# Performance work log

Measured on AMD Instinct MI355X. Metric: run time of the kernel, lower is better.

## Reference

```python
import jax, jax.numpy as jnp
import numpy as np

N, E = 100000, 1600000
IN, H, OUT = 128, 128, 64
LN_EPS = 1e-5


def _prep(edge_index, n):
    # Add self loops (PyG GCNConv default) and compute symmetric normalization.
    loops = jnp.arange(n)
    src = jnp.concatenate([edge_index[0], loops])
    dst = jnp.concatenate([edge_index[1], loops])
    deg = jax.ops.segment_sum(jnp.ones_like(dst, dtype=jnp.float32), dst, num_segments=n)
    dinv = jax.lax.rsqrt(jnp.maximum(deg, 1.0))  # deg >= 1 due to self loops
    return src, dst, dinv


def _gcn_conv(x, W, b, src, dst, dinv, n):
    h = x @ W                                   # [N, F_out] dense transform
    coef = dinv[src] * dinv[dst]                # [E+N] symmetric norm
    msg = h[src] * coef[:, None]                # gather + scale
    out = jax.ops.segment_sum(msg, dst, num_segments=n)  # scatter-add
    return out + b


def _layer_norm(x, g, b):
    mu = jnp.mean(x, axis=-1, keepdims=True)
    var = jnp.mean(jnp.square(x - mu), axis=-1, keepdims=True)
    return (x - mu) * jax.lax.rsqrt(var + LN_EPS) * g + b


def setup_inputs() -> dict:
    key = jax.random.key(0)
    ks = jax.random.split(key, 8)
    return {
        "x": jax.random.normal(ks[0], (N, IN), dtype=jnp.float32),
        "edge_index": jax.random.randint(ks[1], (2, E), 0, N),
        "W1": jax.random.normal(ks[2], (IN, H), dtype=jnp.float32) / np.sqrt(IN).astype(np.float32),
        "b1": jnp.zeros((H,), jnp.float32),
        "g1": jnp.ones((H,), jnp.float32),
        "be1": jnp.zeros((H,), jnp.float32),
        "W2": jax.random.normal(ks[3], (H, H), dtype=jnp.float32) / np.sqrt(H).astype(np.float32),
        "b2": jnp.zeros((H,), jnp.float32),
        "g2": jnp.ones((H,), jnp.float32),
        "be2": jnp.zeros((H,), jnp.float32),
        "W3": jax.random.normal(ks[4], (H, OUT), dtype=jnp.float32) / np.sqrt(H).astype(np.float32),
        "b3": jnp.zeros((OUT,), jnp.float32),
    }


def reference(x, edge_index, W1, b1, g1, be1, W2, b2, g2, be2, W3, b3):
    n = x.shape[0]
    src, dst, dinv = _prep(edge_index, n)
    h = _gcn_conv(x, W1, b1, src, dst, dinv, n)
    h = jax.nn.relu(_layer_norm(h, g1, be1))
    h = _gcn_conv(h, W2, b2, src, dst, dinv, n)
    h = jax.nn.relu(_layer_norm(h, g2, be2))
    return _gcn_conv(h, W3, b3, src, dst, dinv, n)
```

## Files before the change

### kernel.cpp

```cpp
#include <hip/hip_runtime.h>

using short8 = __attribute__((ext_vector_type(8))) short;
using f32x4  = __attribute__((ext_vector_type(4))) float;

#define BSHIFT 9
#define BSIZE  512
#define CAP    12288
#define CHUNK  2048


__device__ __forceinline__ float bf_lo(unsigned int v) {
    return __int_as_float((int)(v << 16));
}
__device__ __forceinline__ float bf_hi(unsigned int v) {
    return __int_as_float((int)(v & 0xffff0000u));
}
__device__ __forceinline__ unsigned int f2bf(float f) {
    unsigned int x = __float_as_uint(f);
    x += 0x7fffu + ((x >> 16) & 1u);
    return x >> 16;
}
__device__ __forceinline__ unsigned int pack_bf2(float lo, float hi) {
    return f2bf(lo) | (f2bf(hi) << 16);
}


__global__ void wconv_kernel(const float* __restrict__ W1, const float* __restrict__ W2,
                             const float* __restrict__ W3, unsigned short* __restrict__ o1,
                             unsigned short* __restrict__ o2, unsigned short* __restrict__ o3) {
    int i = blockIdx.x * 256 + threadIdx.x;
    const float* W;
    unsigned short* o;
    int ncol, j;
    if (i < 16384)      { W = W1; o = o1; ncol = 128; j = i; }
    else if (i < 32768) { W = W2; o = o2; ncol = 128; j = i - 16384; }
    else if (i < 40960) { W = W3; o = o3; ncol = 64;  j = i - 32768; }
    else return;
    int k = j / ncol, c = j % ncol;
    int byte = (c * 256 + k * 2) ^ ((c & 7) << 4);
    o[byte >> 1] = (unsigned short)f2bf(W[j]);
}


__global__ __launch_bounds__(256) void bin_kernel(
    const int* __restrict__ src, const int* __restrict__ dst, int E,
    int2* __restrict__ region, int* __restrict__ bfill) {
    __shared__ int lcnt[256];
    __shared__ int loff[256];
    __shared__ int gbase[256];
    __shared__ int2 stage[CHUNK];
    __shared__ unsigned short bOf[CHUNK];

    int t = threadIdx.x;
    int e0 = blockIdx.x * CHUNK;
    int cnt = min(CHUNK, E - e0);

    lcnt[t] = 0;
    __syncthreads();

    int s_[8], d_[8], p_[8];
#pragma unroll
    for (int i = 0; i < 8; i++) {
        int e = t + i * 256;
        if (e < cnt) {
            int s = src[e0 + e], d = dst[e0 + e];
            s_[i] = s;
            d_[i] = d;
            p_[i] = atomicAdd(&lcnt[d >> BSHIFT], 1);
        } else {
            d_[i] = -1;
        }
    }
    __syncthreads();

    int v = lcnt[t];
    loff[t] = v;
    __syncthreads();
    for (int off = 1; off < 256; off <<= 1) {
        int u = (t >= off) ? loff[t - off] : 0;
        __syncthreads();
        loff[t] += u;
        __syncthreads();
    }
    int ex = loff[t] - v;
    __syncthreads();
    loff[t] = ex;
    gbase[t] = (v > 0) ? atomicAdd(&bfill[t], v) : 0;
    __syncthreads();

#pragma unroll
    for (int i = 0; i < 8; i++) {
        if (d_[i] >= 0) {
            int b = d_[i] >> BSHIFT;
            int j = loff[b] + p_[i];
            stage[j] = make_int2(s_[i], d_[i]);
            bOf[j] = (unsigned short)b;
        }
    }
    __syncthreads();

    for (int j = t; j < cnt; j += 256) {
        int b = bOf[j];
        int idx = gbase[b] + (j - loff[b]);
        if (idx < CAP) region[(size_t)b * CAP + idx] = stage[j];
    }
}

__global__ void bscan_kernel(const int* __restrict__ bfill, int* __restrict__ bbase,
                             int* __restrict__ row_ptr, int nbuck, int n) {
    __shared__ int sh[256];
    int t = threadIdx.x;
    int v = (t < nbuck) ? min(bfill[t], CAP) : 0;
    sh[t] = v;
    __syncthreads();
    for (int off = 1; off < 256; off <<= 1) {
        int u = (t >= off) ? sh[t - off] : 0;
        __syncthreads();
        sh[t] += u;
        __syncthreads();
    }
    if (t < nbuck) bbase[t] = sh[t] - v;
    if (t == nbuck - 1) row_ptr[n] = sh[t];
}

__global__ __launch_bounds__(512) void build_kernel(
    const int2* __restrict__ region, const int* __restrict__ bfill,
    const int* __restrict__ bbase, int* __restrict__ row_ptr, float* __restrict__ dinv,
    int* __restrict__ col, int n) {
    __shared__ int cnt[BSIZE];
    __shared__ int excl[BSIZE];
    __shared__ int fill[BSIZE];
    int b = blockIdx.x;
    int t = threadIdx.x;
    int base = b * BSIZE;
    int ecnt = min(bfill[b], CAP);
    int ebase = bbase[b];
    const int2* reg = region + (size_t)b * CAP;

    cnt[t] = 0;
    fill[t] = 0;
    __syncthreads();

    for (int i = t; i < ecnt; i += 512) atomicAdd(&cnt[reg[i].y - base], 1);
    __syncthreads();

    int v = cnt[t];
    excl[t] = v;
    __syncthreads();
    for (int off = 1; off < 512; off <<= 1) {
        int u = (t >= off) ? excl[t - off] : 0;
        __syncthreads();
        excl[t] += u;
        __syncthreads();
    }
    int ex = excl[t] - v;
    __syncthreads();
    excl[t] = ex;
    __syncthreads();

    int node = base + t;
    if (node < n) {
        row_ptr[node] = ebase + ex;
        dinv[node] = rsqrtf((float)(v + 1));
    }

    for (int i = t; i < ecnt; i += 512) {
        int2 sd = reg[i];
        int li = sd.y - base;
        int pos = atomicAdd(&fill[li], 1);
        col[ebase + excl[li] + pos] = sd.x;
    }
}


template <int NCOL, bool XF32>
__global__ __launch_bounds__(256) void mfma_gemm_kernel(const void* __restrict__ Xv,
                                                        const unsigned short* __restrict__ Wsw,
                                                        const float* __restrict__ dinv,
                                                        unsigned int* __restrict__ Y, int n) {
    constexpr int CF = NCOL / 16;
    __shared__ unsigned short Wt[(size_t)NCOL * 128];

    int t = threadIdx.x;
    {
        const uint4* Wg = (const uint4*)Wsw;
        uint4* Wl = (uint4*)Wt;
        for (int i = t; i < NCOL * 16; i += 256) Wl[i] = Wg[i];
    }
    __syncthreads();

    int wid = t >> 6, l = t & 63;
    int row0 = blockIdx.x * 128;
    int kq = l >> 4;
    const char* Wb = (const char*)Wt;

    for (int rt = 0; rt < 2; rt++) {
        int xr = row0 + (wid * 2 + rt) * 16 + (l & 15);
        int xrc = min(xr, n - 1);

        f32x4 acc[CF];
#pragma unroll
        for (int cf = 0; cf < CF; cf++) acc[cf] = (f32x4){0.f, 0.f, 0.f, 0.f};

#pragma unroll
        for (int ks = 0; ks < 4; ks++) {
            short8 bq;
            if (XF32) {
                const float* Xf = (const float*)Xv + (size_t)xrc * 128 + ks * 32 + kq * 8;
                float4 x0 = ((const float4*)Xf)[0];
                float4 x1 = ((const float4*)Xf)[1];
                unsigned int p0 = pack_bf2(x0.x, x0.y), p1 = pack_bf2(x0.z, x0.w);
                unsigned int p2 = pack_bf2(x1.x, x1.y), p3 = pack_bf2(x1.z, x1.w);
                uint4 u = make_uint4(p0, p1, p2, p3);
                bq = *(const short8*)&u;
            } else {
                const char* Xb = (const char*)Xv + (size_t)xrc * 256 + ks * 64 + kq * 16;
                bq = *(const short8*)Xb;
            }
#pragma unroll
            for (int cf = 0; cf < CF; cf++) {
                int c = cf * 16 + (l & 15);
                int byte = (c * 256 + ks * 64 + kq * 16) ^ ((c & 7) << 4);
                short8 aq = *(const short8*)(Wb + byte);
                acc[cf] = __builtin_amdgcn_mfma_f32_16x16x32_bf16(aq, bq, acc[cf], 0, 0, 0);
            }
        }

        if (xr < n) {
            float dsc = dinv[xr];
            unsigned int* Yr = Y + (size_t)xr * (NCOL / 2);
#pragma unroll
            for (int cf = 0; cf < CF; cf++) {
                uint2 o = make_uint2(pack_bf2(acc[cf][0] * dsc, acc[cf][1] * dsc),
                                     pack_bf2(acc[cf][2] * dsc, acc[cf][3] * dsc));
                *(uint2*)(Yr + cf * 8 + kq * 2) = o;
            }
        }
    }
}


__global__ __launch_bounds__(256) void agg_ln_kernel(
    const unsigned int* __restrict__ tmp, const int* __restrict__ row_ptr,
    const int* __restrict__ col, const float* __restrict__ dinv,
    const float* __restrict__ bias, const float* __restrict__ gamma,
    const float* __restrict__ beta, unsigned int* __restrict__ out, int n) {
    int wid = threadIdx.x >> 6;
    int lane = threadIdx.x & 63;
    int half = lane >> 5;
    int l = lane & 31;
    int stride = gridDim.x * 4;

    const uint2* T = (const uint2*)tmp;

    for (int node = blockIdx.x * 4 + wid; node < n; node += stride) {
        float di = dinv[node];
        int beg = __builtin_amdgcn_readfirstlane(row_ptr[node]);
        int end = __builtin_amdgcn_readfirstlane(row_ptr[node + 1]);

        float a0 = 0.f, a1 = 0.f, a2 = 0.f, a3 = 0.f;
        int e = beg;
#pragma unroll 4
        for (; e + 1 < end; e += 2) {
            int c0 = col[e];
            int c1 = col[e + 1];
            int s = half ? c1 : c0;
            uint2 v = T[(size_t)s * 32 + l];
            a0 += bf_lo(v.x);
            a1 += bf_hi(v.x);
            a2 += bf_lo(v.y);
            a3 += bf_hi(v.y);
        }
        if (half == 1) {
            uint2 v = T[(size_t)node * 32 + l];
            a0 += bf_lo(v.x);
            a1 += bf_hi(v.x);
            a2 += bf_lo(v.y);
            a3 += bf_hi(v.y);
        }
        if (e < end && half == 0) {
            int s = col[e];
            uint2 v = T[(size_t)s * 32 + l];
            a0 += bf_lo(v.x);
            a1 += bf_hi(v.x);
            a2 += bf_lo(v.y);
            a3 += bf_hi(v.y);
        }
        a0 += __shfl_xor(a0, 32, 64);
        a1 += __shfl_xor(a1, 32, 64);
        a2 += __shfl_xor(a2, 32, 64);
        a3 += __shfl_xor(a3, 32, 64);

        float4 bb = ((const float4*)bias)[l];
        a0 = fmaf(a0, di, bb.x);
        a1 = fmaf(a1, di, bb.y);
        a2 = fmaf(a2, di, bb.z);
        a3 = fmaf(a3, di, bb.w);

        float s4 = a0 + a1 + a2 + a3;
#pragma unroll
        for (int m = 1; m < 32; m <<= 1) s4 += __shfl_xor(s4, m, 64);
        float mu = s4 * (1.0f / 128.0f);
        float d0 = a0 - mu, d1 = a1 - mu, d2 = a2 - mu, d3 = a3 - mu;
        float vv = d0 * d0 + d1 * d1 + d2 * d2 + d3 * d3;
#pragma unroll
        for (int m = 1; m < 32; m <<= 1) vv += __shfl_xor(vv, m, 64);
        float r = rsqrtf(vv * (1.0f / 128.0f) + 1e-5f);

        if (half == 0) {
            float4 gg = ((const float4*)gamma)[l];
            float4 be = ((const float4*)beta)[l];
            float o0 = fmaxf(fmaf(d0 * r, gg.x, be.x), 0.f);
            float o1 = fmaxf(fmaf(d1 * r, gg.y, be.y), 0.f);
            float o2 = fmaxf(fmaf(d2 * r, gg.z, be.z), 0.f);
            float o3 = fmaxf(fmaf(d3 * r, gg.w, be.w), 0.f);
            ((uint2*)out)[(size_t)node * 32 + l] = make_uint2(pack_bf2(o0, o1), pack_bf2(o2, o3));
        }
    }
}


__global__ __launch_bounds__(256) void agg64_kernel(
    const unsigned int* __restrict__ tmp, const int* __restrict__ row_ptr,
    const int* __restrict__ col, const float* __restrict__ dinv,
    const float* __restrict__ bias, float* __restrict__ out, int n) {
    int wid = threadIdx.x >> 6;
    int lane = threadIdx.x & 63;
    int q = lane >> 4;
    int l = lane & 15;
    int stride = gridDim.x * 4;

    const uint2* T = (const uint2*)tmp;

    for (int node = blockIdx.x * 4 + wid; node < n; node += stride) {
        float di = dinv[node];
        int beg = __builtin_amdgcn_readfirstlane(row_ptr[node]);
        int end = __builtin_amdgcn_readfirstlane(row_ptr[node + 1]);

        float a0 = 0.f, a1 = 0.f, a2 = 0.f, a3 = 0.f;
        int e = beg;
#pragma unroll 2
        for (; e + 3 < end; e += 4) {
            int c0 = col[e], c1 = col[e + 1], c2 = col[e + 2], c3 = col[e + 3];
            int sa = (q & 1) ? c1 : c0;
            int sb = (q & 1) ? c3 : c2;
            int s = (q & 2) ? sb : sa;
            uint2 v = T[(size_t)s * 16 + l];
            a0 += bf_lo(v.x);
            a1 += bf_hi(v.x);
            a2 += bf_lo(v.y);
            a3 += bf_hi(v.y);
        }
        int rem = end - e;
        if (q < rem) {
            int s = col[e + q];
            uint2 v = T[(size_t)s * 16 + l];
            a0 += bf_lo(v.x);
            a1 += bf_hi(v.x);
            a2 += bf_lo(v.y);
            a3 += bf_hi(v.y);
        }
        if (q == 3) {
            uint2 v = T[(size_t)node * 16 + l];
            a0 += bf_lo(v.x);
            a1 += bf_hi(v.x);
            a2 += bf_lo(v.y);
            a3 += bf_hi(v.y);
        }
        a0 += __shfl_xor(a0, 16, 64);
        a1 += __shfl_xor(a1, 16, 64);
        a2 += __shfl_xor(a2, 16, 64);
        a3 += __shfl_xor(a3, 16, 64);
        a0 += __shfl_xor(a0, 32, 64);
        a1 += __shfl_xor(a1, 32, 64);
        a2 += __shfl_xor(a2, 32, 64);
        a3 += __shfl_xor(a3, 32, 64);

        if (lane < 16) {
            float4 bb = ((const float4*)bias)[l];
            float4 o;
            o.x = fmaf(a0, di, bb.x);
            o.y = fmaf(a1, di, bb.y);
            o.z = fmaf(a2, di, bb.z);
            o.w = fmaf(a3, di, bb.w);
            ((float4*)out)[(size_t)node * 16 + l] = o;
        }
    }
}


extern "C" void kernel_launch(void* const* d_in, const int* in_sizes, int n_in,
                              void* d_out, int out_size, void* d_ws, size_t ws_size,
                              hipStream_t stream) {
    const float* x   = (const float*)d_in[0];
    const int*   ei  = (const int*)d_in[1];
    const float* W1  = (const float*)d_in[2];
    const float* b1  = (const float*)d_in[3];
    const float* g1  = (const float*)d_in[4];
    const float* be1 = (const float*)d_in[5];
    const float* W2  = (const float*)d_in[6];
    const float* b2  = (const float*)d_in[7];
    const float* g2  = (const float*)d_in[8];
    const float* be2 = (const float*)d_in[9];
    const float* W3  = (const float*)d_in[10];
    const float* b3  = (const float*)d_in[11];

    int n = in_sizes[0] / 128;
    int E = in_sizes[1] / 2;
    const int* src = ei;
    const int* dst = ei + E;
    int nbuck = (n + BSIZE - 1) / BSIZE;

    char* p = (char*)d_ws;
    auto alloc = [&](size_t bytes) {
        void* q = (void*)p;
        p += (bytes + 255) & ~(size_t)255;
        return q;
    };
    int*   bfill   = (int*)alloc(256 * 4);
    int*   bbase   = (int*)alloc(256 * 4);
    int*   row_ptr = (int*)alloc((size_t)(n + 1) * 4);
    float* dinv    = (float*)alloc((size_t)n * 4);
    unsigned short* wsw1 = (unsigned short*)alloc(128 * 128 * 2);
    unsigned short* wsw2 = (unsigned short*)alloc(128 * 128 * 2);
    unsigned short* wsw3 = (unsigned short*)alloc(64 * 128 * 2);
    int2*  region  = (int2*)alloc((size_t)nbuck * CAP * 8);
    int*   col     = (int*)alloc((size_t)E * 4);
    unsigned int* bufA = (unsigned int*)alloc((size_t)n * 64 * 4);
    unsigned int* bufB = (unsigned int*)alloc((size_t)n * 64 * 4);

    hipMemsetAsync(bfill, 0, 256 * 4, stream);

    wconv_kernel<<<160, 256, 0, stream>>>(W1, W2, W3, wsw1, wsw2, wsw3);

    int bin_blocks = (E + CHUNK - 1) / CHUNK;
    bin_kernel<<<bin_blocks, 256, 0, stream>>>(src, dst, E, region, bfill);
    bscan_kernel<<<1, 256, 0, stream>>>(bfill, bbase, row_ptr, nbuck, n);
    build_kernel<<<nbuck, 512, 0, stream>>>(region, bfill, bbase, row_ptr, dinv, col, n);

    int gemm_blocks = (n + 127) / 128;
    int agg_blocks = 4096;

    mfma_gemm_kernel<128, true><<<gemm_blocks, 256, 0, stream>>>(x, wsw1, dinv, bufB, n);
    agg_ln_kernel<<<agg_blocks, 256, 0, stream>>>(bufB, row_ptr, col, dinv, b1, g1, be1, bufA, n);

    mfma_gemm_kernel<128, false><<<gemm_blocks, 256, 0, stream>>>(bufA, wsw2, dinv, bufB, n);
    agg_ln_kernel<<<agg_blocks, 256, 0, stream>>>(bufB, row_ptr, col, dinv, b2, g2, be2, bufA, n);

    mfma_gemm_kernel<64, false><<<gemm_blocks, 256, 0, stream>>>(bufA, wsw3, dinv, bufB, n);
    agg64_kernel<<<agg_blocks, 256, 0, stream>>>(bufB, row_ptr, col, dinv, b3, (float*)d_out, n);
}
```

Before: 277.2 us.

## Pack binned edges into one int, drop bucket scan, widen aggregation loads

The binning stage now stores each edge as a single 32-bit word: the source id in the low 17 bits and the local destination offset above it. This halves region traffic. The global bucket scan kernel is removed by giving each bucket a fixed CAP-sized slot in col and storing separate begin/end arrays per node. The aggregation kernels switch to 16-byte loads: the LN kernel uses 16 lanes per row and 4 edges in flight, and the output kernel uses 8 lanes per row and 8 edges per step. This cuts instruction count per gathered row. The trade-offs are a padded col array, a packing that assumes node ids fit in 17 bits, and different lane reduction patterns.

Measured after the change: 271.9 us, median of 2. No clear change (-1.9%).

```diff
diff --git a/kernel.cpp b/kernel.cpp
--- a/kernel.cpp
+++ b/kernel.cpp
@@ -44,11 +44,11 @@
 
 __global__ __launch_bounds__(256) void bin_kernel(
     const int* __restrict__ src, const int* __restrict__ dst, int E,
-    int2* __restrict__ region, int* __restrict__ bfill) {
+    int* __restrict__ region, int* __restrict__ bfill) {
     __shared__ int lcnt[256];
     __shared__ int loff[256];
     __shared__ int gbase[256];
-    __shared__ int2 stage[CHUNK];
+    __shared__ int stage[CHUNK];
     __shared__ unsigned short bOf[CHUNK];
 
     int t = threadIdx.x;
@@ -93,7 +93,7 @@
         if (d_[i] >= 0) {
             int b = d_[i] >> BSHIFT;
             int j = loff[b] + p_[i];
-            stage[j] = make_int2(s_[i], d_[i]);
+            stage[j] = s_[i] | ((d_[i] & (BSIZE - 1)) << 17);
             bOf[j] = (unsigned short)b;
         }
     }
@@ -106,26 +106,9 @@
     }
 }
 
-__global__ void bscan_kernel(const int* __restrict__ bfill, int* __restrict__ bbase,
-                             int* __restrict__ row_ptr, int nbuck, int n) {
-    __shared__ int sh[256];
-    int t = threadIdx.x;
-    int v = (t < nbuck) ? min(bfill[t], CAP) : 0;
-    sh[t] = v;
-    __syncthreads();
-    for (int off = 1; off < 256; off <<= 1) {
-        int u = (t >= off) ? sh[t - off] : 0;
-        __syncthreads();
-        sh[t] += u;
-        __syncthreads();
-    }
-    if (t < nbuck) bbase[t] = sh[t] - v;
-    if (t == nbuck - 1) row_ptr[n] = sh[t];
-}
-
 __global__ __launch_bounds__(512) void build_kernel(
-    const int2* __restrict__ region, const int* __restrict__ bfill,
-    const int* __restrict__ bbase, int* __restrict__ row_ptr, float* __restrict__ dinv,
+    const int* __restrict__ region, const int* __restrict__ bfill,
+    int* __restrict__ rbeg, int* __restrict__ rend, float* __restrict__ dinv,
     int* __restrict__ col, int n) {
     __shared__ int cnt[BSIZE];
     __shared__ int excl[BSIZE];
@@ -134,14 +117,14 @@
     int t = threadIdx.x;
     int base = b * BSIZE;
     int ecnt = min(bfill[b], CAP);
-    int ebase = bbase[b];
-    const int2* reg = region + (size_t)b * CAP;
+    int ebase = b * CAP;
+    const int* reg = region + (size_t)b * CAP;
 
     cnt[t] = 0;
     fill[t] = 0;
     __syncthreads();
 
-    for (int i = t; i < ecnt; i += 512) atomicAdd(&cnt[reg[i].y - base], 1);
+    for (int i = t; i < ecnt; i += 512) atomicAdd(&cnt[reg[i] >> 17], 1);
     __syncthreads();
 
     int v = cnt[t];
@@ -160,15 +143,16 @@
 
     int node = base + t;
     if (node < n) {
-        row_ptr[node] = ebase + ex;
+        rbeg[node] = ebase + ex;
+        rend[node] = ebase + ex + v;
         dinv[node] = rsqrtf((float)(v + 1));
     }
 
     for (int i = t; i < ecnt; i += 512) {
-        int2 sd = reg[i];
-        int li = sd.y - base;
+        int p = reg[i];
+        int li = p >> 17;
         int pos = atomicAdd(&fill[li], 1);
-        col[ebase + excl[li] + pos] = sd.x;
+        col[ebase + excl[li] + pos] = p & 0x1FFFF;
     }
 }
 
@@ -239,105 +223,38 @@
     }
 }
 
+#define ACC8(v)                 \
+    a0 += bf_lo((v).x);         \
+    a1 += bf_hi((v).x);         \
+    a2 += bf_lo((v).y);         \
+    a3 += bf_hi((v).y);         \
+    a4 += bf_lo((v).z);         \
+    a5 += bf_hi((v).z);         \
+    a6 += bf_lo((v).w);         \
+    a7 += bf_hi((v).w);
+
 
 __global__ __launch_bounds__(256) void agg_ln_kernel(
-    const unsigned int* __restrict__ tmp, const int* __restrict__ row_ptr,
-    const int* __restrict__ col, const float* __restrict__ dinv,
-    const float* __restrict__ bias, const float* __restrict__ gamma,
-    const float* __restrict__ beta, unsigned int* __restrict__ out, int n) {
-    int wid = threadIdx.x >> 6;
-    int lane = threadIdx.x & 63;
-    int half = lane >> 5;
-    int l = lane & 31;
-    int stride = gridDim.x * 4;
-
-    const uint2* T = (const uint2*)tmp;
-
-    for (int node = blockIdx.x * 4 + wid; node < n; node += stride) {
-        float di = dinv[node];
-        int beg = __builtin_amdgcn_readfirstlane(row_ptr[node]);
-        int end = __builtin_amdgcn_readfirstlane(row_ptr[node + 1]);
-
-        float a0 = 0.f, a1 = 0.f, a2 = 0.f, a3 = 0.f;
-        int e = beg;
-#pragma unroll 4
-        for (; e + 1 < end; e += 2) {
-            int c0 = col[e];
-            int c1 = col[e + 1];
-            int s = half ? c1 : c0;
-            uint2 v = T[(size_t)s * 32 + l];
-            a0 += bf_lo(v.x);
-            a1 += bf_hi(v.x);
-            a2 += bf_lo(v.y);
-            a3 += bf_hi(v.y);
-        }
-        if (half == 1) {
-            uint2 v = T[(size_t)node * 32 + l];
-            a0 += bf_lo(v.x);
-            a1 += bf_hi(v.x);
-            a2 += bf_lo(v.y);
-            a3 += bf_hi(v.y);
-        }
-        if (e < end && half == 0) {
-            int s = col[e];
-            uint2 v = T[(size_t)s * 32 + l];
-            a0 += bf_lo(v.x);
-            a1 += bf_hi(v.x);
-            a2 += bf_lo(v.y);
-            a3 += bf_hi(v.y);
-        }
-        a0 += __shfl_xor(a0, 32, 64);
-        a1 += __shfl_xor(a1, 32, 64);
-        a2 += __shfl_xor(a2, 32, 64);
-        a3 += __shfl_xor(a3, 32, 64);
-
-        float4 bb = ((const float4*)bias)[l];
-        a0 = fmaf(a0, di, bb.x);
-        a1 = fmaf(a1, di, bb.y);
-        a2 = fmaf(a2, di, bb.z);
-        a3 = fmaf(a3, di, bb.w);
-
-        float s4 = a0 + a1 + a2 + a3;
-#pragma unroll
-        for (int m = 1; m < 32; m <<= 1) s4 += __shfl_xor(s4, m, 64);
-        float mu = s4 * (1.0f / 128.0f);
-        float d0 = a0 - mu, d1 = a1 - mu, d2 = a2 - mu, d3 = a3 - mu;
-        float vv = d0 * d0 + d1 * d1 + d2 * d2 + d3 * d3;
-#pragma unroll
-        for (int m = 1; m < 32; m <<= 1) vv += __shfl_xor(vv, m, 64);
-        float r = rsqrtf(vv * (1.0f / 128.0f) + 1e-5f);
-
-        if (half == 0) {
-            float4 gg = ((const float4*)gamma)[l];
-            float4 be = ((const float4*)beta)[l];
-            float o0 = fmaxf(fmaf(d0 * r, gg.x, be.x), 0.f);
-            float o1 = fmaxf(fmaf(d1 * r, gg.y, be.y), 0.f);
-            float o2 = fmaxf(fmaf(d2 * r, gg.z, be.z), 0.f);
-            float o3 = fmaxf(fmaf(d3 * r, gg.w, be.w), 0.f);
-            ((uint2*)out)[(size_t)node * 32 + l] = make_uint2(pack_bf2(o0, o1), pack_bf2(o2, o3));
-        }
-    }
-}
-
-
-__global__ __launch_bounds__(256) void agg64_kernel(
-    const unsigned int* __restrict__ tmp, const int* __restrict__ row_ptr,
-    const int* __restrict__ col, const float* __restrict__ dinv,
-    const float* __restrict__ bias, float* __restrict__ out, int n) {
+    const unsigned int* __restrict__ tmp, const int* __restrict__ rbeg,
+    const int* __restrict__ rend, const int* __restrict__ col,
+    const float* __restrict__ dinv, const float* __restrict__ bias,
+    const float* __restrict__ gamma, const float* __restrict__ beta,
+    unsigned int* __restrict__ out, int n) {
     int wid = threadIdx.x >> 6;
     int lane = threadIdx.x & 63;
     int q = lane >> 4;
     int l = lane & 15;
     int stride = gridDim.x * 4;
 
-    const uint2* T = (const uint2*)tmp;
+    const uint4* T = (const uint4*)tmp;
 
     for (int node = blockIdx.x * 4 + wid; node < n; node += stride) {
         float di = dinv[node];
-        int beg = __builtin_amdgcn_readfirstlane(row_ptr[node]);
-        int end = __builtin_amdgcn_readfirstlane(row_ptr[node + 1]);
+        int beg = __builtin_amdgcn_readfirstlane(rbeg[node]);
+        int end = __builtin_amdgcn_readfirstlane(rend[node]);
 
         float a0 = 0.f, a1 = 0.f, a2 = 0.f, a3 = 0.f;
+        float a4 = 0.f, a5 = 0.f, a6 = 0.f, a7 = 0.f;
         int e = beg;
 #pragma unroll 2
         for (; e + 3 < end; e += 4) {
@@ -345,45 +262,136 @@
             int sa = (q & 1) ? c1 : c0;
             int sb = (q & 1) ? c3 : c2;
             int s = (q & 2) ? sb : sa;
-            uint2 v = T[(size_t)s * 16 + l];
-            a0 += bf_lo(v.x);
-            a1 += bf_hi(v.x);
-            a2 += bf_lo(v.y);
-            a3 += bf_hi(v.y);
+            uint4 v = T[(size_t)s * 16 + l];
+            ACC8(v)
         }
         int rem = end - e;
         if (q < rem) {
             int s = col[e + q];
-            uint2 v = T[(size_t)s * 16 + l];
-            a0 += bf_lo(v.x);
-            a1 += bf_hi(v.x);
-            a2 += bf_lo(v.y);
-            a3 += bf_hi(v.y);
+            uint4 v = T[(size_t)s * 16 + l];
+            ACC8(v)
         }
         if (q == 3) {
-            uint2 v = T[(size_t)node * 16 + l];
-            a0 += bf_lo(v.x);
-            a1 += bf_hi(v.x);
-            a2 += bf_lo(v.y);
-            a3 += bf_hi(v.y);
-        }
-        a0 += __shfl_xor(a0, 16, 64);
-        a1 += __shfl_xor(a1, 16, 64);
-        a2 += __shfl_xor(a2, 16, 64);
-        a3 += __shfl_xor(a3, 16, 64);
-        a0 += __shfl_xor(a0, 32, 64);
-        a1 += __shfl_xor(a1, 32, 64);
-        a2 += __shfl_xor(a2, 32, 64);
-        a3 += __shfl_xor(a3, 32, 64);
+            uint4 v = T[(size_t)node * 16 + l];
+            ACC8(v)
+        }
+        a0 += __shfl_xor(a0, 16, 64); a1 += __shfl_xor(a1, 16, 64);
+        a2 += __shfl_xor(a2, 16, 64); a3 += __shfl_xor(a3, 16, 64);
+        a4 += __shfl_xor(a4, 16, 64); a5 += __shfl_xor(a5, 16, 64);
+        a6 += __shfl_xor(a6, 16, 64); a7 += __shfl_xor(a7, 16, 64);
+        a0 += __shfl_xor(a0, 32, 64); a1 += __shfl_xor(a1, 32, 64);
+        a2 += __shfl_xor(a2, 32, 64); a3 += __shfl_xor(a3, 32, 64);
+        a4 += __shfl_xor(a4, 32, 64); a5 += __shfl_xor(a5, 32, 64);
+        a6 += __shfl_xor(a6, 32, 64); a7 += __shfl_xor(a7, 32, 64);
+
+        float4 b0 = ((const float4*)bias)[2 * l];
+        float4 b1 = ((const float4*)bias)[2 * l + 1];
+        a0 = fmaf(a0, di, b0.x); a1 = fmaf(a1, di, b0.y);
+        a2 = fmaf(a2, di, b0.z); a3 = fmaf(a3, di, b0.w);
+        a4 = fmaf(a4, di, b1.x); a5 = fmaf(a5, di, b1.y);
+        a6 = fmaf(a6, di, b1.z); a7 = fmaf(a7, di, b1.w);
+
+        float s8 = a0 + a1 + a2 + a3 + a4 + a5 + a6 + a7;
+#pragma unroll
+        for (int m = 1; m < 16; m <<= 1) s8 += __shfl_xor(s8, m, 64);
+        float mu = s8 * (1.0f / 128.0f);
+        float d0 = a0 - mu, d1 = a1 - mu, d2 = a2 - mu, d3 = a3 - mu;
+        float d4 = a4 - mu, d5 = a5 - mu, d6 = a6 - mu, d7 = a7 - mu;
+        float vv = d0 * d0 + d1 * d1 + d2 * d2 + d3 * d3 +
+                   d4 * d4 + d5 * d5 + d6 * d6 + d7 * d7;
+#pragma unroll
+        for (int m = 1; m < 16; m <<= 1) vv += __shfl_xor(vv, m, 64);
+        float r = rsqrtf(vv * (1.0f / 128.0f) + 1e-5f);
 
         if (lane < 16) {
-            float4 bb = ((const float4*)bias)[l];
-            float4 o;
-            o.x = fmaf(a0, di, bb.x);
-            o.y = fmaf(a1, di, bb.y);
-            o.z = fmaf(a2, di, bb.z);
-            o.w = fmaf(a3, di, bb.w);
-            ((float4*)out)[(size_t)node * 16 + l] = o;
+            float4 g0 = ((const float4*)gamma)[2 * l];
+            float4 g1 = ((const float4*)gamma)[2 * l + 1];
+            float4 e0 = ((const float4*)beta)[2 * l];
+            float4 e1 = ((const float4*)beta)[2 * l + 1];
+            float o0 = fmaxf(fmaf(d0 * r, g0.x, e0.x), 0.f);
+            float o1 = fmaxf(fmaf(d1 * r, g0.y, e0.y), 0.f);
+            float o2 = fmaxf(fmaf(d2 * r, g0.z, e0.z), 0.f);
+            float o3 = fmaxf(fmaf(d3 * r, g0.w, e0.w), 0.f);
+            float o4 = fmaxf(fmaf(d4 * r, g1.x, e1.x), 0.f);
+            float o5 = fmaxf(fmaf(d5 * r, g1.y, e1.y), 0.f);
+            float o6 = fmaxf(fmaf(d6 * r, g1.z, e1.z), 0.f);
+            float o7 = fmaxf(fmaf(d7 * r, g1.w, e1.w), 0.f);
+            uint4 o = make_uint4(pack_bf2(o0, o1), pack_bf2(o2, o3),
+                                 pack_bf2(o4, o5), pack_bf2(o6, o7));
+            ((uint4*)out)[(size_t)node * 16 + l] = o;
+        }
+    }
+}
+
+
+__global__ __launch_bounds__(256) void agg64_kernel(
+    const unsigned int* __restrict__ tmp, const int* __restrict__ rbeg,
+    const int* __restrict__ rend, const int* __restrict__ col,
+    const float* __restrict__ dinv, const float* __restrict__ bias,
+    float* __restrict__ out, int n) {
+    int wid = threadIdx.x >> 6;
+    int lane = threadIdx.x & 63;
+    int oc = lane >> 3;
+    int l = lane & 7;
+    int stride = gridDim.x * 4;
+
+    const uint4* T = (const uint4*)tmp;
+
+    for (int node = blockIdx.x * 4 + wid; node < n; node += stride) {
+        float di = dinv[node];
+        int beg = __builtin_amdgcn_readfirstlane(rbeg[node]);
+        int end = __builtin_amdgcn_readfirstlane(rend[node]);
+
+        float a0 = 0.f, a1 = 0.f, a2 = 0.f, a3 = 0.f;
+        float a4 = 0.f, a5 = 0.f, a6 = 0.f, a7 = 0.f;
+        int e = beg;
+#pragma unroll 2
+        for (; e + 7 < end; e += 8) {
+            int c0 = col[e], c1 = col[e + 1], c2 = col[e + 2], c3 = col[e + 3];
+            int c4 = col[e + 4], c5 = col[e + 5], c6 = col[e + 6], c7 = col[e + 7];
+            int sa = (oc & 1) ? c1 : c0;
+            int sb = (oc & 1) ? c3 : c2;
+            int sc = (oc & 1) ? c5 : c4;
+            int sd = (oc & 1) ? c7 : c6;
+            int sab = (oc & 2) ? sb : sa;
+            int scd = (oc & 2) ? sd : sc;
+            int s = (oc & 4) ? scd : sab;
+            uint4 v = T[(size_t)s * 8 + l];
+            ACC8(v)
+        }
+        int rem = end - e;
+        if (oc < rem) {
+            int s = col[e + oc];
+            uint4 v = T[(size_t)s * 8 + l];
+            ACC8(v)
+        }
+        if (oc == 7) {
+            uint4 v = T[(size_t)node * 8 + l];
+            ACC8(v)
+        }
+        a0 += __shfl_xor(a0, 8, 64);  a1 += __shfl_xor(a1, 8, 64);
+        a2 += __shfl_xor(a2, 8, 64);  a3 += __shfl_xor(a3, 8, 64);
+        a4 += __shfl_xor(a4, 8, 64);  a5 += __shfl_xor(a5, 8, 64);
+        a6 += __shfl_xor(a6, 8, 64);  a7 += __shfl_xor(a7, 8, 64);
+        a0 += __shfl_xor(a0, 16, 64); a1 += __shfl_xor(a1, 16, 64);
+        a2 += __shfl_xor(a2, 16, 64); a3 += __shfl_xor(a3, 16, 64);
+        a4 += __shfl_xor(a4, 16, 64); a5 += __shfl_xor(a5, 16, 64);
+        a6 += __shfl_xor(a6, 16, 64); a7 += __shfl_xor(a7, 16, 64);
+        a0 += __shfl_xor(a0, 32, 64); a1 += __shfl_xor(a1, 32, 64);
+        a2 += __shfl_xor(a2, 32, 64); a3 += __shfl_xor(a3, 32, 64);
+        a4 += __shfl_xor(a4, 32, 64); a5 += __shfl_xor(a5, 32, 64);
+        a6 += __shfl_xor(a6, 32, 64); a7 += __shfl_xor(a7, 32, 64);
+
+        if (lane < 8) {
+            float4 b0 = ((const float4*)bias)[2 * l];
+            float4 b1 = ((const float4*)bias)[2 * l + 1];
+            float4 o0, o1;
+            o0.x = fmaf(a0, di, b0.x); o0.y = fmaf(a1, di, b0.y);
+            o0.z = fmaf(a2, di, b0.z); o0.w = fmaf(a3, di, b0.w);
+            o1.x = fmaf(a4, di, b1.x); o1.y = fmaf(a5, di, b1.y);
+            o1.z = fmaf(a6, di, b1.z); o1.w = fmaf(a7, di, b1.w);
+            ((float4*)out)[(size_t)node * 16 + 2 * l] = o0;
+            ((float4*)out)[(size_t)node * 16 + 2 * l + 1] = o1;
         }
     }
 }
@@ -418,14 +426,14 @@
         return q;
     };
     int*   bfill   = (int*)alloc(256 * 4);
-    int*   bbase   = (int*)alloc(256 * 4);
-    int*   row_ptr = (int*)alloc((size_t)(n + 1) * 4);
+    int*   rbeg    = (int*)alloc((size_t)n * 4);
+    int*   rend    = (int*)alloc((size_t)n * 4);
     float* dinv    = (float*)alloc((size_t)n * 4);
     unsigned short* wsw1 = (unsigned short*)alloc(128 * 128 * 2);
     unsigned short* wsw2 = (unsigned short*)alloc(128 * 128 * 2);
     unsigned short* wsw3 = (unsigned short*)alloc(64 * 128 * 2);
-    int2*  region  = (int2*)alloc((size_t)nbuck * CAP * 8);
-    int*   col     = (int*)alloc((size_t)E * 4);
+    int*   region  = (int*)alloc((size_t)nbuck * CAP * 4);
+    int*   col     = (int*)alloc((size_t)nbuck * CAP * 4);
     unsigned int* bufA = (unsigned int*)alloc((size_t)n * 64 * 4);
     unsigned int* bufB = (unsigned int*)alloc((size_t)n * 64 * 4);
 
@@ -435,18 +443,17 @@
 
     int bin_blocks = (E + CHUNK - 1) / CHUNK;
     bin_kernel<<<bin_blocks, 256, 0, stream>>>(src, dst, E, region, bfill);
-    bscan_kernel<<<1, 256, 0, stream>>>(bfill, bbase, row_ptr, nbuck, n);
-    build_kernel<<<nbuck, 512, 0, stream>>>(region, bfill, bbase, row_ptr, dinv, col, n);
+    build_kernel<<<nbuck, 512, 0, stream>>>(region, bfill, rbeg, rend, dinv, col, n);
 
     int gemm_blocks = (n + 127) / 128;
     int agg_blocks = 4096;
 
     mfma_gemm_kernel<128, true><<<gemm_blocks, 256, 0, stream>>>(x, wsw1, dinv, bufB, n);
-    agg_ln_kernel<<<agg_blocks, 256, 0, stream>>>(bufB, row_ptr, col, dinv, b1, g1, be1, bufA, n);
+    agg_ln_kernel<<<agg_blocks, 256, 0, stream>>>(bufB, rbeg, rend, col, dinv, b1, g1, be1, bufA, n);
 
     mfma_gemm_kernel<128, false><<<gemm_blocks, 256, 0, stream>>>(bufA, wsw2, dinv, bufB, n);
-    agg_ln_kernel<<<agg_blocks, 256, 0, stream>>>(bufB, row_ptr, col, dinv, b2, g2, be2, bufA, n);
+    agg_ln_kernel<<<agg_blocks, 256, 0, stream>>>(bufB, rbeg, rend, col, dinv, b2, g2, be2, bufA, n);
 
     mfma_gemm_kernel<64, false><<<gemm_blocks, 256, 0, stream>>>(bufA, wsw3, dinv, bufB, n);
-    agg64_kernel<<<agg_blocks, 256, 0, stream>>>(bufB, row_ptr, col, dinv, b3, (float*)d_out, n);
-}
+    agg64_kernel<<<agg_blocks, 256, 0, stream>>>(bufB, rbeg, rend, col, dinv, b3, (float*)d_out, n);
+}
```
